# Performance work log

Hardware: AMD Instinct MI355X
Metric: run time of the kernel (lower is better)

## Reference

```python
import jax, jax.numpy as jnp
import numpy as np

INPUT_DIM = 41      # observed channels
D = 2 * INPUT_DIM   # attention value dim (values + mask concat)
E = 128             # embed_time
NH = 1              # num_heads
DK = E // NH
H = 128             # nhidden
NLIN = 50
LAT = 20
B, TK, TQ = 8, 512, 128


def _lin_init(k, out_d, in_d):
    return jax.random.normal(k, (out_d, in_d)) * (1.0 / np.sqrt(in_d))


def setup_inputs() -> dict:
    key = jax.random.key(0)
    ks = jax.random.split(key, 32)
    vals = jax.random.normal(ks[0], (B, TK, INPUT_DIM))
    obs = (jax.random.uniform(ks[1], (B, TK, INPUT_DIM)) > 0.3).astype(jnp.float32)
    x = jnp.concatenate([vals * obs, obs], axis=-1)          # [B,TK,2*INPUT_DIM]
    time_steps = jnp.sort(jax.random.uniform(ks[2], (B, TK)), axis=1)
    query = jnp.linspace(0.0, 1.0, TQ)                        # reference time points
    inp = dict(x=x, time_steps=time_steps, query=query)
    # learned time embedders (mtan_time_embedder): Linear(1,1) + Linear(1,E-1)
    inp['e1_wp'] = jax.random.normal(ks[3], (E - 1,)); inp['e1_bp'] = jax.random.normal(ks[4], (E - 1,)) * 0.1
    inp['e1_wl'] = jax.random.normal(ks[5], (1,));     inp['e1_bl'] = jax.random.normal(ks[6], (1,)) * 0.1
    inp['e2_wp'] = jax.random.normal(ks[7], (E - 1,)); inp['e2_bp'] = jax.random.normal(ks[8], (E - 1,)) * 0.1
    inp['e2_wl'] = jax.random.normal(ks[9], (1,));     inp['e2_bl'] = jax.random.normal(ks[10], (1,)) * 0.1
    # multiTimeAttention linears
    inp['Wq'] = _lin_init(ks[11], E, E); inp['bq'] = jnp.zeros((E,))
    inp['Wk'] = _lin_init(ks[12], E, E); inp['bk'] = jnp.zeros((E,))
    inp['Wo'] = _lin_init(ks[13], H, NH * D); inp['bo'] = jnp.zeros((H,))
    # bidirectional GRU (PyTorch layout: W_ih [3H,in], W_hh [3H,H])
    inp['gwi_f'] = _lin_init(ks[14], 3 * H, H); inp['gwh_f'] = _lin_init(ks[15], 3 * H, H)
    inp['gbi_f'] = jnp.zeros((3 * H,));         inp['gbh_f'] = jnp.zeros((3 * H,))
    inp['gwi_b'] = _lin_init(ks[16], 3 * H, H); inp['gwh_b'] = _lin_init(ks[17], 3 * H, H)
    inp['gbi_b'] = jnp.zeros((3 * H,));         inp['gbh_b'] = jnp.zeros((3 * H,))
    # hiddens_to_z0 MLP
    inp['W1'] = _lin_init(ks[18], NLIN, 2 * H); inp['b1'] = jnp.zeros((NLIN,))
    inp['W2'] = _lin_init(ks[19], 2 * LAT, NLIN); inp['b2'] = jnp.zeros((2 * LAT,))
    return inp


def _time_embed(tt, wp, bp, wl, bl):
    tt = tt[..., None]                               # [...,1]
    out1 = tt * wl + bl                              # [...,1]
    out2 = jnp.sin(tt * wp + bp)                     # [...,E-1]
    return jnp.concatenate([out1, out2], axis=-1)    # [...,E]


def _gru_scan(xs, Wi, Wh, bi, bh):
    # xs: [T,B,in] -> hidden states [T,B,H]; PyTorch GRU equations
    h0 = jnp.zeros((xs.shape[1], Wh.shape[1]), xs.dtype)
    def step(h, xt):
        gi = xt @ Wi.T + bi
        gh = h @ Wh.T + bh
        ir, iz, inn = jnp.split(gi, 3, axis=-1)
        hr, hz, hn = jnp.split(gh, 3, axis=-1)
        r = jax.nn.sigmoid(ir + hr)
        z = jax.nn.sigmoid(iz + hz)
        n = jnp.tanh(inn + r * hn)
        hnew = (1.0 - z) * n + z * h
        return hnew, hnew
    _, ys = jax.lax.scan(step, h0, xs)
    return ys


def reference(x, time_steps, query, e1_wp, e1_bp, e1_wl, e1_bl, e2_wp, e2_bp, e2_wl, e2_bl,
              Wq, bq, Wk, bk, Wo, bo, gwi_f, gwh_f, gbi_f, gbh_f, gwi_b, gwh_b, gbi_b, gbh_b,
              W1, b1, W2, b2):
    b, tk, _ = x.shape
    tq = query.shape[0]
    mask = x[:, :, INPUT_DIM:]                                 # [B,TK,INPUT_DIM]
    mask2 = jnp.concatenate([mask, mask], axis=-1)             # [B,TK,D]
    k_emb = _time_embed(time_steps, e1_wp, e1_bp, e1_wl, e1_bl)   # embedder1(key)   [B,TK,E]
    q_emb = _time_embed(query[None, :], e2_wp, e2_bp, e2_wl, e2_bl)  # embedder2(query) [1,TQ,E]
    q = (q_emb @ Wq.T + bq).reshape(1, tq, NH, DK).transpose(0, 2, 1, 3)   # [1,h,TQ,dk]
    k = (k_emb @ Wk.T + bk).reshape(b, tk, NH, DK).transpose(0, 2, 1, 3)   # [B,h,TK,dk]
    scores = jnp.einsum('ahqd,bhkd->bhqk', q, k) / np.sqrt(DK)             # [B,h,TQ,TK]
    # per-channel masked softmax over keys (the blown-up 5D tensor in the original)
    s5 = jnp.where(mask2[:, None, None, :, :] == 0, -1e9, scores[..., None])  # [B,h,TQ,TK,D]
    p = jax.nn.softmax(s5, axis=-2)
    att = jnp.einsum('bhqkd,bkd->bhqd', p, x)                  # value = x; [B,h,TQ,D]
    att = att.transpose(0, 2, 1, 3).reshape(b, tq, NH * D)
    out = att @ Wo.T + bo                                      # [B,TQ,H]
    xs = out.transpose(1, 0, 2)                                # [TQ,B,H]
    hf = _gru_scan(xs, gwi_f, gwh_f, gbi_f, gbh_f)
    hb = _gru_scan(xs[::-1], gwi_b, gwh_b, gbi_b, gbh_b)[::-1]
    h = jnp.concatenate([hf, hb], axis=-1).transpose(1, 0, 2)  # [B,TQ,2H]
    z = jax.nn.relu(h @ W1.T + b1) @ W2.T + b2                 # [B,TQ,2*LAT]
    return z
```

## Files before the change

kernel.cpp:

```cpp
#include <hip/hip_runtime.h>
#include <math.h>

#define TKK 512
#define TQQ 128
#define BB  8
#define EE  128
#define DD  82
#define IND 41
#define HH  128
#define G3  384
#define NL  50
#define OD  40

typedef __attribute__((ext_vector_type(8))) short short8v;
typedef __attribute__((ext_vector_type(4))) float f32x4;
#define MFMA16(a, b, c) __builtin_amdgcn_mfma_f32_16x16x32_bf16(a, b, c, 0, 0, 0)
#define RCP(x) __builtin_amdgcn_rcpf(x)

__device__ __forceinline__ short f2bf(float f) {
  unsigned u = __float_as_uint(f);
  unsigned r = (u + 0x7fffu + ((u >> 16) & 1u)) >> 16;
  return (short)r;
}
__device__ __forceinline__ float dot4(float4 a, float4 b) {
  return a.x * b.x + a.y * b.y + a.z * b.z + a.w * b.w;
}

__global__ __launch_bounds__(128) void embed_project(
    const float* __restrict__ time_steps, const float* __restrict__ query,
    const float* __restrict__ e1_wp, const float* __restrict__ e1_bp,
    const float* __restrict__ e1_wl, const float* __restrict__ e1_bl,
    const float* __restrict__ e2_wp, const float* __restrict__ e2_bp,
    const float* __restrict__ e2_wl, const float* __restrict__ e2_bl,
    const float* __restrict__ Wk, const float* __restrict__ bk,
    const float* __restrict__ Wq, const float* __restrict__ bq,
    float* __restrict__ kproj, float* __restrict__ qproj) {
  __shared__ float emb[8][EE];
  int i = blockIdx.x;
  int e = threadIdx.x;
  const float *wp, *bp, *wl, *bl, *W, *bias;
  float* out;
  int row0;
  const float* tsrc;
  if (i < 512) {
    int b = i & 7, rg = i >> 3;
    row0 = b * TKK + rg * 8;
    tsrc = time_steps + row0;
    wp = e1_wp; bp = e1_bp; wl = e1_wl; bl = e1_bl; W = Wk; bias = bk;
    out = kproj + (size_t)row0 * EE;
  } else {
    int qg = i - 512;
    row0 = qg * 8;
    tsrc = query + row0;
    wp = e2_wp; bp = e2_bp; wl = e2_wl; bl = e2_bl; W = Wq; bias = bq;
    out = qproj + (size_t)row0 * EE;
  }
  float wpv = 0.f, bpv = 0.f;
  if (e > 0) { wpv = wp[e - 1]; bpv = bp[e - 1]; }
  float wlv = wl[0], blv = bl[0];
#pragma unroll
  for (int r = 0; r < 8; r++) {
    float t = tsrc[r];
    emb[r][e] = (e == 0) ? (t * wlv + blv) : sinf(t * wpv + bpv);
  }
  __syncthreads();
  const float4* wr4 = (const float4*)(W + (size_t)e * EE);
  const float4* em4 = (const float4*)emb;
  float bv = bias[e];
  float acc[8];
#pragma unroll
  for (int r = 0; r < 8; r++) acc[r] = bv;
#pragma unroll 4
  for (int c = 0; c < 32; c++) {
    float4 wv = wr4[c];
#pragma unroll
    for (int r = 0; r < 8; r++) acc[r] += dot4(wv, em4[r * 32 + c]);
  }
#pragma unroll
  for (int r = 0; r < 8; r++) out[(size_t)r * EE + e] = acc[r];
}

__global__ __launch_bounds__(256) void attention(
    const float* __restrict__ x, const float* __restrict__ kproj,
    const float* __restrict__ qproj, const float* __restrict__ Wo,
    const float* __restrict__ bo,
    const float* __restrict__ gwi_f, const float* __restrict__ gbi_f,
    const float* __restrict__ gwi_b, const float* __restrict__ gbi_b,
    float* __restrict__ gi) {
  __shared__ float qv[4][EE];
  __shared__ float4 w4[TKK];
  __shared__ float red[4][4];
  __shared__ float mfin[4];
  __shared__ float part[2][4][DD];
  __shared__ float numb[4][DD];
  __shared__ float attb[4][DD];
  __shared__ float xsr[4][EE];
  __shared__ float wo_lds[HH * DD];
  int b = blockIdx.x & 7, qg = blockIdx.x >> 3;
  int q0 = qg * 4;
  int tid = threadIdx.x;
  int rq = tid >> 2, ec = tid & 3;

  {
    int idx = tid * 2, qi = idx >> 7, j = idx & 127;
    *(float2*)&qv[qi][j] = *(const float2*)(qproj + (size_t)(q0 + qi) * EE + j);
    const float4* wo4 = (const float4*)Wo;
    float4* wl4 = (float4*)wo_lds;
#pragma unroll
    for (int it = 0; it < 11; it++) {
      int i4 = tid + it * 256;
      if (i4 < HH * DD / 4) wl4[i4] = wo4[i4];
    }
  }
  __syncthreads();

  const float scale = 0.08838834764831845f;
  float lm[4] = {-1e30f, -1e30f, -1e30f, -1e30f};
  const float4* qv4 = (const float4*)qv;
  for (int p = 0; p < 8; p++) {
    int r = p * 64 + rq;
    const float4* kr = (const float4*)(kproj + (size_t)(b * TKK + r) * EE);
    float s[4] = {0.f, 0.f, 0.f, 0.f};
#pragma unroll
    for (int c = 0; c < 8; c++) {
      float4 kv = kr[c * 4 + ec];
#pragma unroll
      for (int qi = 0; qi < 4; qi++) s[qi] += dot4(kv, qv4[qi * 32 + c * 4 + ec]);
    }
#pragma unroll
    for (int qi = 0; qi < 4; qi++) {
      s[qi] += __shfl_xor(s[qi], 1, 64);
      s[qi] += __shfl_xor(s[qi], 2, 64);
      s[qi] *= scale;
      lm[qi] = fmaxf(lm[qi], s[qi]);
    }
    if (ec == 0) { float4 sv = {s[0], s[1], s[2], s[3]}; w4[r] = sv; }
  }
  for (int off = 32; off; off >>= 1)
#pragma unroll
    for (int qi = 0; qi < 4; qi++) lm[qi] = fmaxf(lm[qi], __shfl_xor(lm[qi], off, 64));
  if ((tid & 63) == 0)
#pragma unroll
    for (int qi = 0; qi < 4; qi++) red[tid >> 6][qi] = lm[qi];
  __syncthreads();
  if (tid < 4) {
    float m = red[0][tid];
    for (int w = 1; w < 4; w++) m = fmaxf(m, red[w][tid]);
    mfin[tid] = m;
  }
  __syncthreads();
  {
    float m0 = mfin[0], m1 = mfin[1], m2 = mfin[2], m3 = mfin[3];
    float4 v0 = w4[tid], v1 = w4[256 + tid];
    v0.x = __expf(v0.x - m0); v0.y = __expf(v0.y - m1);
    v0.z = __expf(v0.z - m2); v0.w = __expf(v0.w - m3);
    v1.x = __expf(v1.x - m0); v1.y = __expf(v1.y - m1);
    v1.z = __expf(v1.z - m2); v1.w = __expf(v1.w - m3);
    w4[tid] = v0; w4[256 + tid] = v1;
  }
  __syncthreads();

  if (tid < 2 * DD) {
    int c = (tid >= DD), d = tid - c * DD;
    const float* xp = x + ((size_t)(b * TKK + c * 256)) * DD + d;
    float a0 = 0.f, a1 = 0.f, a2 = 0.f, a3 = 0.f;
#pragma unroll 8
    for (int k = 0; k < 256; k++) {
      float xv = xp[(size_t)k * DD];
      float4 wv = w4[c * 256 + k];
      a0 += wv.x * xv; a1 += wv.y * xv; a2 += wv.z * xv; a3 += wv.w * xv;
    }
    part[c][0][d] = a0; part[c][1][d] = a1; part[c][2][d] = a2; part[c][3][d] = a3;
  }
  __syncthreads();
  if (tid < DD) {
#pragma unroll
    for (int qi = 0; qi < 4; qi++) numb[qi][tid] = part[0][qi][tid] + part[1][qi][tid];
  }
  __syncthreads();
  if (tid < DD) {
    int j = tid % IND;
#pragma unroll
    for (int qi = 0; qi < 4; qi++)
      attb[qi][tid] = numb[qi][tid] * RCP(numb[qi][IND + j]);
  }
  __syncthreads();

  {
    int o = tid & 127, g = tid >> 7;
    const float* wrow = wo_lds + o * DD;
    float acc0 = bo[o], acc1 = acc0;
#pragma unroll 2
    for (int d = 0; d < DD; d++) {
      float wv = wrow[d];
      acc0 += wv * attb[2 * g][d];
      acc1 += wv * attb[2 * g + 1][d];
    }
    xsr[2 * g][o] = acc0;
    xsr[2 * g + 1][o] = acc1;
  }
  __syncthreads();

  const float4* xs4 = (const float4*)xsr;
  for (int p = 0; p < 12; p++) {
    int o = p * 64 + rq;
    int dirn = (o >= G3) ? 1 : 0;
    int oo = o - dirn * G3;
    int gate = oo >> 7, col = oo & 127;
    const float4* wr = (const float4*)((dirn ? gwi_b : gwi_f) + (size_t)oo * EE);
    float a[4] = {0.f, 0.f, 0.f, 0.f};
#pragma unroll
    for (int c = 0; c < 8; c++) {
      float4 wv = wr[c * 4 + ec];
#pragma unroll
      for (int qi = 0; qi < 4; qi++) a[qi] += dot4(wv, xs4[qi * 32 + c * 4 + ec]);
    }
#pragma unroll
    for (int qi = 0; qi < 4; qi++) {
      a[qi] += __shfl_xor(a[qi], 1, 64);
      a[qi] += __shfl_xor(a[qi], 2, 64);
    }
    float bi = (dirn ? gbi_b : gbi_f)[oo];
    if (ec == 0) {
      float* gp = gi + (((size_t)(dirn * BB + b) * TQQ + q0) * HH + col) * 4 + gate;
      gp[0] = a[0] + bi; gp[512] = a[1] + bi; gp[1024] = a[2] + bi; gp[1536] = a[3] + bi;
    }
  }
}

__global__ __launch_bounds__(512, 1) void gru_seq(const float* __restrict__ gi,
                                                  const float* __restrict__ gwh_f,
                                                  const float* __restrict__ gbh_f,
                                                  const float* __restrict__ gwh_b,
                                                  const float* __restrict__ gbh_b,
                                                  float* __restrict__ hcat) {
  __shared__ short hb[2][HH];
  int dir = blockIdx.x >> 3, b = blockIdx.x & 7;
  const float* Wh = dir ? gwh_b : gwh_f;
  const float* bh = dir ? gbh_b : gbh_f;
  int tid = threadIdx.x;
  int w = tid >> 6, l = tid & 63;
  int lhi = l >> 4, llo = l & 15;
  int o = 16 * w + llo;
  bool tl = (lhi == 0);

  for (int i = tid; i < 2 * HH / 2; i += 512) ((int*)hb)[i] = 0;

  short8v Bf[3][4];
#pragma unroll
  for (int g = 0; g < 3; g++) {
    const float* wr = Wh + (size_t)(g * HH + o) * EE;
#pragma unroll
    for (int kk = 0; kk < 4; kk++) {
      int k0 = kk * 32 + lhi * 8;
      short8v v;
#pragma unroll
      for (int i = 0; i < 8; i++) v[i] = f2bf(wr[k0 + i]);
      Bf[g][kk] = v;
    }
  }
  float bhr = bh[o], bhz = bh[HH + o], bhn = bh[2 * HH + o];
  float hprev = 0.f;
  float hst[16];

  float4 g0, g1, g2, g3;
  const size_t dbase = ((size_t)(dir * BB + b) * TQQ) * 512 + (size_t)o * 4;

  auto gi_load = [&](int step, float4& dst) {
    int tt = dir ? (TQQ - 1 - step) : step;
    dst = *(const float4*)(gi + dbase + (size_t)tt * 512);
  };
  __syncthreads();
  gi_load(0, g0); gi_load(1, g1);

  auto body = [&](int step, float4& gc, float4& gn, float& hs) {
    int cur = step & 1;
    const char* hrow = (const char*)&hb[cur][0];
    int ao = lhi * 16;
    short8v A0 = *(const short8v*)(hrow + 0 * 64 + ao);
    short8v A1 = *(const short8v*)(hrow + 1 * 64 + ao);
    short8v A2 = *(const short8v*)(hrow + 2 * 64 + ao);
    short8v A3 = *(const short8v*)(hrow + 3 * 64 + ao);
    { int ls = step + 2; gi_load(ls > TQQ - 1 ? TQQ - 1 : ls, gn); }
    f32x4 z4 = {0.f, 0.f, 0.f, 0.f};
    f32x4 aR = z4, aZ = z4, aN = z4;
    aR = MFMA16(A0, Bf[0][0], aR); aZ = MFMA16(A0, Bf[1][0], aZ); aN = MFMA16(A0, Bf[2][0], aN);
    aR = MFMA16(A1, Bf[0][1], aR); aZ = MFMA16(A1, Bf[1][1], aZ); aN = MFMA16(A1, Bf[2][1], aN);
    aR = MFMA16(A2, Bf[0][2], aR); aZ = MFMA16(A2, Bf[1][2], aZ); aN = MFMA16(A2, Bf[2][2], aN);
    aR = MFMA16(A3, Bf[0][3], aR); aZ = MFMA16(A3, Bf[1][3], aZ); aN = MFMA16(A3, Bf[2][3], aN);
    if (tl) {
      float rp = gc.x + bhr + aR[0];
      float zp = gc.y + bhz + aZ[0];
      float hn = aN[0] + bhn;
      float r = RCP(1.f + __expf(-rp));
      float z = RCP(1.f + __expf(-zp));
      float a = gc.z + r * hn;
      float e = __expf(2.f * a);
      float n = 1.f - 2.f * RCP(1.f + e);
      float hnew = n + z * (hprev - n);
      hprev = hnew;
      hs = hnew;
      hb[cur ^ 1][o] = f2bf(hnew);
    }
    asm volatile("s_waitcnt lgkmcnt(0)" ::: "memory");
    __builtin_amdgcn_s_barrier();
    __builtin_amdgcn_sched_barrier(0);
  };

  for (int so = 0; so < TQQ / 16; so++) {
    int s0i = so * 16;
    body(s0i + 0,  g0, g2, hst[0]);
    body(s0i + 1,  g1, g3, hst[1]);
    body(s0i + 2,  g2, g0, hst[2]);
    body(s0i + 3,  g3, g1, hst[3]);
    body(s0i + 4,  g0, g2, hst[4]);
    body(s0i + 5,  g1, g3, hst[5]);
    body(s0i + 6,  g2, g0, hst[6]);
    body(s0i + 7,  g3, g1, hst[7]);
    body(s0i + 8,  g0, g2, hst[8]);
    body(s0i + 9,  g1, g3, hst[9]);
    body(s0i + 10, g2, g0, hst[10]);
    body(s0i + 11, g3, g1, hst[11]);
    body(s0i + 12, g0, g2, hst[12]);
    body(s0i + 13, g1, g3, hst[13]);
    body(s0i + 14, g2, g0, hst[14]);
    body(s0i + 15, g3, g1, hst[15]);
    if (tl) {
#pragma unroll
      for (int si = 0; si < 16; si++) {
        int step = s0i + si;
        int t = dir ? (TQQ - 1 - step) : step;
        hcat[((size_t)b * TQQ + t) * (2 * HH) + dir * HH + o] = hst[si];
      }
    }
  }
}

__global__ __launch_bounds__(512) void mlp_out(const float* __restrict__ hcat,
                                               const float* __restrict__ W1,
                                               const float* __restrict__ b1,
                                               const float* __restrict__ W2,
                                               const float* __restrict__ b2,
                                               float* __restrict__ out) {
  __shared__ float hrow[8][2 * HH];
  __shared__ float ybuf[8][52];
  int i = blockIdx.x;
  int b = i & 7, tg = i >> 3;
  int tid = threadIdx.x;
  size_t rowbase = (size_t)(b * TQQ + tg * 8) * (2 * HH);
  ((float4*)hrow)[tid] = *(const float4*)(hcat + rowbase + tid * 4);
  __syncthreads();
  int r = tid >> 6, o = tid & 63;
  if (o < NL) {
    const float4* w1 = (const float4*)(W1 + (size_t)o * (2 * HH));
    const float4* h4 = (const float4*)hrow[r];
    float acc = b1[o];
#pragma unroll 8
    for (int c = 0; c < 64; c++) acc += dot4(w1[c], h4[c]);
    ybuf[r][o] = fmaxf(acc, 0.f);
  }
  __syncthreads();
  if (o < OD) {
    const float* w2 = W2 + (size_t)o * NL;
    float acc = b2[o];
#pragma unroll 10
    for (int j = 0; j < NL; j++) acc += w2[j] * ybuf[r][j];
    out[((size_t)(b * TQQ + tg * 8) + r) * OD + o] = acc;
  }
}

extern "C" void kernel_launch(void* const* d_in, const int* in_sizes, int n_in,
                              void* d_out, int out_size, void* d_ws, size_t ws_size,
                              hipStream_t stream) {
  const float* x          = (const float*)d_in[0];
  const float* time_steps = (const float*)d_in[1];
  const float* query      = (const float*)d_in[2];
  const float* e1_wp = (const float*)d_in[3];
  const float* e1_bp = (const float*)d_in[4];
  const float* e1_wl = (const float*)d_in[5];
  const float* e1_bl = (const float*)d_in[6];
  const float* e2_wp = (const float*)d_in[7];
  const float* e2_bp = (const float*)d_in[8];
  const float* e2_wl = (const float*)d_in[9];
  const float* e2_bl = (const float*)d_in[10];
  const float* Wq = (const float*)d_in[11];
  const float* bq = (const float*)d_in[12];
  const float* Wk = (const float*)d_in[13];
  const float* bk = (const float*)d_in[14];
  const float* Wo = (const float*)d_in[15];
  const float* bo = (const float*)d_in[16];
  const float* gwi_f = (const float*)d_in[17];
  const float* gwh_f = (const float*)d_in[18];
  const float* gbi_f = (const float*)d_in[19];
  const float* gbh_f = (const float*)d_in[20];
  const float* gwi_b = (const float*)d_in[21];
  const float* gwh_b = (const float*)d_in[22];
  const float* gbi_b = (const float*)d_in[23];
  const float* gbh_b = (const float*)d_in[24];
  const float* W1 = (const float*)d_in[25];
  const float* b1 = (const float*)d_in[26];
  const float* W2 = (const float*)d_in[27];
  const float* b2 = (const float*)d_in[28];

  float* ws    = (float*)d_ws;
  float* kproj = ws;
  float* qproj = kproj + 4096 * 128;
  float* gi    = qproj + 128 * 128;
  float* hcat  = gi + 16 * 128 * 128 * 4;

  embed_project<<<528, 128, 0, stream>>>(time_steps, query,
                                         e1_wp, e1_bp, e1_wl, e1_bl,
                                         e2_wp, e2_bp, e2_wl, e2_bl,
                                         Wk, bk, Wq, bq, kproj, qproj);
  attention<<<256, 256, 0, stream>>>(x, kproj, qproj, Wo, bo,
                                     gwi_f, gbi_f, gwi_b, gbi_b, gi);
  gru_seq<<<16, 512, 0, stream>>>(gi, gwh_f, gbh_f, gwh_b, gbh_b, hcat);
  mlp_out<<<128, 512, 0, stream>>>(hcat, W1, b1, W2, b2, (float*)d_out);
}
```

Baseline: 104.8 us.

## Double attention block threads and halve GRU waves with two column tiles each

The attention kernel now runs 512 threads per block. Score, value-reduction, output-projection and gate loops are re-split across twice as many threads, and the value reduction is split into four key chunks. The GRU kernel goes from 8 to 4 waves, each wave computing two 16-column MFMA tiles. More lanes do useful gate math, barrier cost per step should drop, and the gi prefetch distance grows to three steps. The trade-off is more registers per wave in the GRU (twice the B fragments) and an extra partial-sum reduction in attention.

Result: faster. 99.84 us (-4.7%).

```diff
diff --git a/kernel.cpp b/kernel.cpp
--- a/kernel.cpp
+++ b/kernel.cpp
@@ -80,7 +80,7 @@
   for (int r = 0; r < 8; r++) out[(size_t)r * EE + e] = acc[r];
 }
 
-__global__ __launch_bounds__(256) void attention(
+__global__ __launch_bounds__(512) void attention(
     const float* __restrict__ x, const float* __restrict__ kproj,
     const float* __restrict__ qproj, const float* __restrict__ Wo,
     const float* __restrict__ bo,
@@ -89,9 +89,9 @@
     float* __restrict__ gi) {
   __shared__ float qv[4][EE];
   __shared__ float4 w4[TKK];
-  __shared__ float red[4][4];
+  __shared__ float red[8][4];
   __shared__ float mfin[4];
-  __shared__ float part[2][4][DD];
+  __shared__ float part[4][4][DD];
   __shared__ float numb[4][DD];
   __shared__ float attb[4][DD];
   __shared__ float xsr[4][EE];
@@ -102,13 +102,12 @@
   int rq = tid >> 2, ec = tid & 3;
 
   {
-    int idx = tid * 2, qi = idx >> 7, j = idx & 127;
-    *(float2*)&qv[qi][j] = *(const float2*)(qproj + (size_t)(q0 + qi) * EE + j);
+    qv[tid >> 7][tid & 127] = qproj[(size_t)(q0 + (tid >> 7)) * EE + (tid & 127)];
     const float4* wo4 = (const float4*)Wo;
     float4* wl4 = (float4*)wo_lds;
 #pragma unroll
-    for (int it = 0; it < 11; it++) {
-      int i4 = tid + it * 256;
+    for (int it = 0; it < 6; it++) {
+      int i4 = tid + it * 512;
       if (i4 < HH * DD / 4) wl4[i4] = wo4[i4];
     }
   }
@@ -117,8 +116,8 @@
   const float scale = 0.08838834764831845f;
   float lm[4] = {-1e30f, -1e30f, -1e30f, -1e30f};
   const float4* qv4 = (const float4*)qv;
-  for (int p = 0; p < 8; p++) {
-    int r = p * 64 + rq;
+  for (int p = 0; p < 4; p++) {
+    int r = p * 128 + rq;
     const float4* kr = (const float4*)(kproj + (size_t)(b * TKK + r) * EE);
     float s[4] = {0.f, 0.f, 0.f, 0.f};
 #pragma unroll
@@ -145,37 +144,39 @@
   __syncthreads();
   if (tid < 4) {
     float m = red[0][tid];
-    for (int w = 1; w < 4; w++) m = fmaxf(m, red[w][tid]);
+#pragma unroll
+    for (int w = 1; w < 8; w++) m = fmaxf(m, red[w][tid]);
     mfin[tid] = m;
   }
   __syncthreads();
   {
     float m0 = mfin[0], m1 = mfin[1], m2 = mfin[2], m3 = mfin[3];
-    float4 v0 = w4[tid], v1 = w4[256 + tid];
+    float4 v0 = w4[tid];
     v0.x = __expf(v0.x - m0); v0.y = __expf(v0.y - m1);
     v0.z = __expf(v0.z - m2); v0.w = __expf(v0.w - m3);
-    v1.x = __expf(v1.x - m0); v1.y = __expf(v1.y - m1);
-    v1.z = __expf(v1.z - m2); v1.w = __expf(v1.w - m3);
-    w4[tid] = v0; w4[256 + tid] = v1;
-  }
-  __syncthreads();
-
-  if (tid < 2 * DD) {
-    int c = (tid >= DD), d = tid - c * DD;
-    const float* xp = x + ((size_t)(b * TKK + c * 256)) * DD + d;
-    float a0 = 0.f, a1 = 0.f, a2 = 0.f, a3 = 0.f;
+    w4[tid] = v0;
+  }
+  __syncthreads();
+
+  {
+    int c2 = tid >> 7, d = tid & 127;
+    if (d < DD) {
+      const float* xp = x + ((size_t)(b * TKK + c2 * 128)) * DD + d;
+      float a0 = 0.f, a1 = 0.f, a2 = 0.f, a3 = 0.f;
 #pragma unroll 8
-    for (int k = 0; k < 256; k++) {
-      float xv = xp[(size_t)k * DD];
-      float4 wv = w4[c * 256 + k];
-      a0 += wv.x * xv; a1 += wv.y * xv; a2 += wv.z * xv; a3 += wv.w * xv;
-    }
-    part[c][0][d] = a0; part[c][1][d] = a1; part[c][2][d] = a2; part[c][3][d] = a3;
+      for (int k = 0; k < 128; k++) {
+        float xv = xp[(size_t)k * DD];
+        float4 wv = w4[c2 * 128 + k];
+        a0 += wv.x * xv; a1 += wv.y * xv; a2 += wv.z * xv; a3 += wv.w * xv;
+      }
+      part[c2][0][d] = a0; part[c2][1][d] = a1; part[c2][2][d] = a2; part[c2][3][d] = a3;
+    }
   }
   __syncthreads();
   if (tid < DD) {
 #pragma unroll
-    for (int qi = 0; qi < 4; qi++) numb[qi][tid] = part[0][qi][tid] + part[1][qi][tid];
+    for (int qi = 0; qi < 4; qi++)
+      numb[qi][tid] = part[0][qi][tid] + part[1][qi][tid] + part[2][qi][tid] + part[3][qi][tid];
   }
   __syncthreads();
   if (tid < DD) {
@@ -189,21 +190,16 @@
   {
     int o = tid & 127, g = tid >> 7;
     const float* wrow = wo_lds + o * DD;
-    float acc0 = bo[o], acc1 = acc0;
+    float acc = bo[o];
 #pragma unroll 2
-    for (int d = 0; d < DD; d++) {
-      float wv = wrow[d];
-      acc0 += wv * attb[2 * g][d];
-      acc1 += wv * attb[2 * g + 1][d];
-    }
-    xsr[2 * g][o] = acc0;
-    xsr[2 * g + 1][o] = acc1;
+    for (int d = 0; d < DD; d++) acc += wrow[d] * attb[g][d];
+    xsr[g][o] = acc;
   }
   __syncthreads();
 
   const float4* xs4 = (const float4*)xsr;
-  for (int p = 0; p < 12; p++) {
-    int o = p * 64 + rq;
+  for (int p = 0; p < 6; p++) {
+    int o = p * 128 + rq;
     int dirn = (o >= G3) ? 1 : 0;
     int oo = o - dirn * G3;
     int gate = oo >> 7, col = oo & 127;
@@ -228,7 +224,7 @@
   }
 }
 
-__global__ __launch_bounds__(512, 1) void gru_seq(const float* __restrict__ gi,
+__global__ __launch_bounds__(256, 1) void gru_seq(const float* __restrict__ gi,
                                                   const float* __restrict__ gwh_f,
                                                   const float* __restrict__ gbh_f,
                                                   const float* __restrict__ gwh_b,
@@ -241,37 +237,43 @@
   int tid = threadIdx.x;
   int w = tid >> 6, l = tid & 63;
   int lhi = l >> 4, llo = l & 15;
-  int o = 16 * w + llo;
-  bool tl = (lhi == 0);
-
-  for (int i = tid; i < 2 * HH / 2; i += 512) ((int*)hb)[i] = 0;
-
-  short8v Bf[3][4];
-#pragma unroll
-  for (int g = 0; g < 3; g++) {
-    const float* wr = Wh + (size_t)(g * HH + o) * EE;
-#pragma unroll
-    for (int kk = 0; kk < 4; kk++) {
-      int k0 = kk * 32 + lhi * 8;
-      short8v v;
-#pragma unroll
-      for (int i = 0; i < 8; i++) v[i] = f2bf(wr[k0 + i]);
-      Bf[g][kk] = v;
-    }
-  }
-  float bhr = bh[o], bhz = bh[HH + o], bhn = bh[2 * HH + o];
+  int col0 = 32 * w + llo, col1 = col0 + 16;
+  bool c0 = (lhi < 2);
+  int o_sel = c0 ? col0 : col1;
+  bool wr_lane = ((lhi & 1) == 0);
+
+  if (tid < HH) { hb[0][tid] = 0; hb[1][tid] = 0; }
+
+  short8v Bf[2][3][4];
+#pragma unroll
+  for (int tj = 0; tj < 2; tj++) {
+    int colt = 32 * w + 16 * tj + llo;
+#pragma unroll
+    for (int g = 0; g < 3; g++) {
+      const float* wrp = Wh + (size_t)(g * HH + colt) * EE;
+#pragma unroll
+      for (int kk = 0; kk < 4; kk++) {
+        int k0 = kk * 32 + lhi * 8;
+        short8v v;
+#pragma unroll
+        for (int i = 0; i < 8; i++) v[i] = f2bf(wrp[k0 + i]);
+        Bf[tj][g][kk] = v;
+      }
+    }
+  }
+  float bhr = bh[o_sel], bhz = bh[HH + o_sel], bhn = bh[2 * HH + o_sel];
   float hprev = 0.f;
   float hst[16];
 
   float4 g0, g1, g2, g3;
-  const size_t dbase = ((size_t)(dir * BB + b) * TQQ) * 512 + (size_t)o * 4;
+  const size_t dbase = ((size_t)(dir * BB + b) * TQQ) * 512 + (size_t)o_sel * 4;
 
   auto gi_load = [&](int step, float4& dst) {
     int tt = dir ? (TQQ - 1 - step) : step;
     dst = *(const float4*)(gi + dbase + (size_t)tt * 512);
   };
   __syncthreads();
-  gi_load(0, g0); gi_load(1, g1);
+  gi_load(0, g0); gi_load(1, g1); gi_load(2, g2);
 
   auto body = [&](int step, float4& gc, float4& gn, float& hs) {
     int cur = step & 1;
@@ -281,27 +283,32 @@
     short8v A1 = *(const short8v*)(hrow + 1 * 64 + ao);
     short8v A2 = *(const short8v*)(hrow + 2 * 64 + ao);
     short8v A3 = *(const short8v*)(hrow + 3 * 64 + ao);
-    { int ls = step + 2; gi_load(ls > TQQ - 1 ? TQQ - 1 : ls, gn); }
+    { int ls = step + 3; gi_load(ls > TQQ - 1 ? TQQ - 1 : ls, gn); }
     f32x4 z4 = {0.f, 0.f, 0.f, 0.f};
-    f32x4 aR = z4, aZ = z4, aN = z4;
-    aR = MFMA16(A0, Bf[0][0], aR); aZ = MFMA16(A0, Bf[1][0], aZ); aN = MFMA16(A0, Bf[2][0], aN);
-    aR = MFMA16(A1, Bf[0][1], aR); aZ = MFMA16(A1, Bf[1][1], aZ); aN = MFMA16(A1, Bf[2][1], aN);
-    aR = MFMA16(A2, Bf[0][2], aR); aZ = MFMA16(A2, Bf[1][2], aZ); aN = MFMA16(A2, Bf[2][2], aN);
-    aR = MFMA16(A3, Bf[0][3], aR); aZ = MFMA16(A3, Bf[1][3], aZ); aN = MFMA16(A3, Bf[2][3], aN);
-    if (tl) {
-      float rp = gc.x + bhr + aR[0];
-      float zp = gc.y + bhz + aZ[0];
-      float hn = aN[0] + bhn;
-      float r = RCP(1.f + __expf(-rp));
-      float z = RCP(1.f + __expf(-zp));
-      float a = gc.z + r * hn;
-      float e = __expf(2.f * a);
-      float n = 1.f - 2.f * RCP(1.f + e);
-      float hnew = n + z * (hprev - n);
-      hprev = hnew;
-      hs = hnew;
-      hb[cur ^ 1][o] = f2bf(hnew);
-    }
+    f32x4 aR0 = z4, aZ0 = z4, aN0 = z4, aR1 = z4, aZ1 = z4, aN1 = z4;
+    aR0 = MFMA16(A0, Bf[0][0][0], aR0); aZ0 = MFMA16(A0, Bf[0][1][0], aZ0); aN0 = MFMA16(A0, Bf[0][2][0], aN0);
+    aR1 = MFMA16(A0, Bf[1][0][0], aR1); aZ1 = MFMA16(A0, Bf[1][1][0], aZ1); aN1 = MFMA16(A0, Bf[1][2][0], aN1);
+    aR0 = MFMA16(A1, Bf[0][0][1], aR0); aZ0 = MFMA16(A1, Bf[0][1][1], aZ0); aN0 = MFMA16(A1, Bf[0][2][1], aN0);
+    aR1 = MFMA16(A1, Bf[1][0][1], aR1); aZ1 = MFMA16(A1, Bf[1][1][1], aZ1); aN1 = MFMA16(A1, Bf[1][2][1], aN1);
+    aR0 = MFMA16(A2, Bf[0][0][2], aR0); aZ0 = MFMA16(A2, Bf[0][1][2], aZ0); aN0 = MFMA16(A2, Bf[0][2][2], aN0);
+    aR1 = MFMA16(A2, Bf[1][0][2], aR1); aZ1 = MFMA16(A2, Bf[1][1][2], aZ1); aN1 = MFMA16(A2, Bf[1][2][2], aN1);
+    aR0 = MFMA16(A3, Bf[0][0][3], aR0); aZ0 = MFMA16(A3, Bf[0][1][3], aZ0); aN0 = MFMA16(A3, Bf[0][2][3], aN0);
+    aR1 = MFMA16(A3, Bf[1][0][3], aR1); aZ1 = MFMA16(A3, Bf[1][1][3], aZ1); aN1 = MFMA16(A3, Bf[1][2][3], aN1);
+    float rs = c0 ? aR0[0] : aR1[0];
+    float zs = c0 ? aZ0[0] : aZ1[0];
+    float ns = c0 ? aN0[0] : aN1[0];
+    float rp = gc.x + bhr + rs;
+    float zp = gc.y + bhz + zs;
+    float hn = ns + bhn;
+    float r = RCP(1.f + __expf(-rp));
+    float z = RCP(1.f + __expf(-zp));
+    float a = gc.z + r * hn;
+    float e = __expf(2.f * a);
+    float n = 1.f - 2.f * RCP(1.f + e);
+    float hnew = n + z * (hprev - n);
+    hprev = hnew;
+    hs = hnew;
+    if (wr_lane) hb[cur ^ 1][o_sel] = f2bf(hnew);
     asm volatile("s_waitcnt lgkmcnt(0)" ::: "memory");
     __builtin_amdgcn_s_barrier();
     __builtin_amdgcn_sched_barrier(0);
@@ -309,28 +316,28 @@
 
   for (int so = 0; so < TQQ / 16; so++) {
     int s0i = so * 16;
-    body(s0i + 0,  g0, g2, hst[0]);
-    body(s0i + 1,  g1, g3, hst[1]);
-    body(s0i + 2,  g2, g0, hst[2]);
-    body(s0i + 3,  g3, g1, hst[3]);
-    body(s0i + 4,  g0, g2, hst[4]);
-    body(s0i + 5,  g1, g3, hst[5]);
-    body(s0i + 6,  g2, g0, hst[6]);
-    body(s0i + 7,  g3, g1, hst[7]);
-    body(s0i + 8,  g0, g2, hst[8]);
-    body(s0i + 9,  g1, g3, hst[9]);
-    body(s0i + 10, g2, g0, hst[10]);
-    body(s0i + 11, g3, g1, hst[11]);
-    body(s0i + 12, g0, g2, hst[12]);
-    body(s0i + 13, g1, g3, hst[13]);
-    body(s0i + 14, g2, g0, hst[14]);
-    body(s0i + 15, g3, g1, hst[15]);
-    if (tl) {
+    body(s0i + 0,  g0, g3, hst[0]);
+    body(s0i + 1,  g1, g0, hst[1]);
+    body(s0i + 2,  g2, g1, hst[2]);
+    body(s0i + 3,  g3, g2, hst[3]);
+    body(s0i + 4,  g0, g3, hst[4]);
+    body(s0i + 5,  g1, g0, hst[5]);
+    body(s0i + 6,  g2, g1, hst[6]);
+    body(s0i + 7,  g3, g2, hst[7]);
+    body(s0i + 8,  g0, g3, hst[8]);
+    body(s0i + 9,  g1, g0, hst[9]);
+    body(s0i + 10, g2, g1, hst[10]);
+    body(s0i + 11, g3, g2, hst[11]);
+    body(s0i + 12, g0, g3, hst[12]);
+    body(s0i + 13, g1, g0, hst[13]);
+    body(s0i + 14, g2, g1, hst[14]);
+    body(s0i + 15, g3, g2, hst[15]);
+    if (wr_lane) {
 #pragma unroll
       for (int si = 0; si < 16; si++) {
         int step = s0i + si;
         int t = dir ? (TQQ - 1 - step) : step;
-        hcat[((size_t)b * TQQ + t) * (2 * HH) + dir * HH + o] = hst[si];
+        hcat[((size_t)b * TQQ + t) * (2 * HH) + dir * HH + o_sel] = hst[si];
       }
     }
   }
@@ -412,8 +419,8 @@
                                          e1_wp, e1_bp, e1_wl, e1_bl,
                                          e2_wp, e2_bp, e2_wl, e2_bl,
                                          Wk, bk, Wq, bq, kproj, qproj);
-  attention<<<256, 256, 0, stream>>>(x, kproj, qproj, Wo, bo,
+  attention<<<256, 512, 0, stream>>>(x, kproj, qproj, Wo, bo,
                                      gwi_f, gbi_f, gwi_b, gbi_b, gi);
-  gru_seq<<<16, 512, 0, stream>>>(gi, gwh_f, gbh_f, gwh_b, gbh_b, hcat);
+  gru_seq<<<16, 256, 0, stream>>>(gi, gwh_f, gbh_f, gwh_b, gbh_b, hcat);
   mlp_out<<<128, 512, 0, stream>>>(hcat, W1, b1, W2, b2, (float*)d_out);
 }
```

## Store keys, x and GRU input weights in bf16 and widen attention blocks

Applied to the files above, without the earlier changes.

Adds a conversion kernel that casts x and the GRU input weights to bf16, and makes embed_project write the key projections in bf16. The attention kernel now reads these half-width buffers, unpacking to fp32 for the math, and runs 512 threads per block with the key, x and gate loops split across twice as many threads. The aim is to cut global memory traffic in the attention stage and raise parallelism per block. The cost is an extra kernel launch plus a full pass over x every call, and reduced precision in scores and gate inputs.

New measurement: 106.6 us. No clear change (+1.8%).

```diff
diff --git a/kernel.cpp b/kernel.cpp
--- a/kernel.cpp
+++ b/kernel.cpp
@@ -22,8 +22,25 @@
   unsigned r = (u + 0x7fffu + ((u >> 16) & 1u)) >> 16;
   return (short)r;
 }
+__device__ __forceinline__ float bl(unsigned u) { return __uint_as_float(u << 16); }
+__device__ __forceinline__ float bh(unsigned u) { return __uint_as_float(u & 0xffff0000u); }
 __device__ __forceinline__ float dot4(float4 a, float4 b) {
   return a.x * b.x + a.y * b.y + a.z * b.z + a.w * b.w;
+}
+
+__global__ __launch_bounds__(512) void to_bf16(const float* __restrict__ x,
+                                               const float* __restrict__ gwi_f,
+                                               const float* __restrict__ gwi_b,
+                                               unsigned short* __restrict__ x_bf,
+                                               unsigned short* __restrict__ gwi_bf) {
+  int idx = blockIdx.x * 512 + threadIdx.x;
+  if (idx < 335872) {
+    x_bf[idx] = (unsigned short)f2bf(x[idx]);
+  } else {
+    int j = idx - 335872;
+    float v = (j < 49152) ? gwi_f[j] : gwi_b[j - 49152];
+    gwi_bf[j] = (unsigned short)f2bf(v);
+  }
 }
 
 __global__ __launch_bounds__(128) void embed_project(
@@ -34,26 +51,24 @@
     const float* __restrict__ e2_wl, const float* __restrict__ e2_bl,
     const float* __restrict__ Wk, const float* __restrict__ bk,
     const float* __restrict__ Wq, const float* __restrict__ bq,
-    float* __restrict__ kproj, float* __restrict__ qproj) {
+    unsigned short* __restrict__ kproj_bf, float* __restrict__ qproj) {
   __shared__ float emb[8][EE];
   int i = blockIdx.x;
   int e = threadIdx.x;
   const float *wp, *bp, *wl, *bl, *W, *bias;
-  float* out;
   int row0;
   const float* tsrc;
-  if (i < 512) {
+  bool kside = (i < 512);
+  if (kside) {
     int b = i & 7, rg = i >> 3;
     row0 = b * TKK + rg * 8;
     tsrc = time_steps + row0;
     wp = e1_wp; bp = e1_bp; wl = e1_wl; bl = e1_bl; W = Wk; bias = bk;
-    out = kproj + (size_t)row0 * EE;
   } else {
     int qg = i - 512;
     row0 = qg * 8;
     tsrc = query + row0;
     wp = e2_wp; bp = e2_bp; wl = e2_wl; bl = e2_bl; W = Wq; bias = bq;
-    out = qproj + (size_t)row0 * EE;
   }
   float wpv = 0.f, bpv = 0.f;
   if (e > 0) { wpv = wp[e - 1]; bpv = bp[e - 1]; }
@@ -76,22 +91,29 @@
 #pragma unroll
     for (int r = 0; r < 8; r++) acc[r] += dot4(wv, em4[r * 32 + c]);
   }
-#pragma unroll
-  for (int r = 0; r < 8; r++) out[(size_t)r * EE + e] = acc[r];
-}
-
-__global__ __launch_bounds__(256) void attention(
-    const float* __restrict__ x, const float* __restrict__ kproj,
+  if (kside) {
+#pragma unroll
+    for (int r = 0; r < 8; r++)
+      kproj_bf[(size_t)(row0 + r) * EE + e] = (unsigned short)f2bf(acc[r]);
+  } else {
+#pragma unroll
+    for (int r = 0; r < 8; r++) qproj[(size_t)(row0 + r) * EE + e] = acc[r];
+  }
+}
+
+__global__ __launch_bounds__(512) void attention(
+    const unsigned short* __restrict__ x_bf,
+    const unsigned short* __restrict__ kproj_bf,
     const float* __restrict__ qproj, const float* __restrict__ Wo,
     const float* __restrict__ bo,
-    const float* __restrict__ gwi_f, const float* __restrict__ gbi_f,
-    const float* __restrict__ gwi_b, const float* __restrict__ gbi_b,
+    const unsigned short* __restrict__ gwi_bf,
+    const float* __restrict__ gbi_f, const float* __restrict__ gbi_b,
     float* __restrict__ gi) {
   __shared__ float qv[4][EE];
   __shared__ float4 w4[TKK];
-  __shared__ float red[4][4];
+  __shared__ float red[8][4];
   __shared__ float mfin[4];
-  __shared__ float part[2][4][DD];
+  __shared__ float part[4][4][DD];
   __shared__ float numb[4][DD];
   __shared__ float attb[4][DD];
   __shared__ float xsr[4][EE];
@@ -102,13 +124,12 @@
   int rq = tid >> 2, ec = tid & 3;
 
   {
-    int idx = tid * 2, qi = idx >> 7, j = idx & 127;
-    *(float2*)&qv[qi][j] = *(const float2*)(qproj + (size_t)(q0 + qi) * EE + j);
+    qv[tid >> 7][tid & 127] = qproj[(size_t)(q0 + (tid >> 7)) * EE + (tid & 127)];
     const float4* wo4 = (const float4*)Wo;
     float4* wl4 = (float4*)wo_lds;
 #pragma unroll
-    for (int it = 0; it < 11; it++) {
-      int i4 = tid + it * 256;
+    for (int it = 0; it < 6; it++) {
+      int i4 = tid + it * 512;
       if (i4 < HH * DD / 4) wl4[i4] = wo4[i4];
     }
   }
@@ -117,15 +138,23 @@
   const float scale = 0.08838834764831845f;
   float lm[4] = {-1e30f, -1e30f, -1e30f, -1e30f};
   const float4* qv4 = (const float4*)qv;
-  for (int p = 0; p < 8; p++) {
-    int r = p * 64 + rq;
-    const float4* kr = (const float4*)(kproj + (size_t)(b * TKK + r) * EE);
+  for (int p = 0; p < 4; p++) {
+    int r = p * 128 + rq;
+    const uint4* kr = (const uint4*)(kproj_bf + (size_t)(b * TKK + r) * EE);
     float s[4] = {0.f, 0.f, 0.f, 0.f};
 #pragma unroll
-    for (int c = 0; c < 8; c++) {
-      float4 kv = kr[c * 4 + ec];
-#pragma unroll
-      for (int qi = 0; qi < 4; qi++) s[qi] += dot4(kv, qv4[qi * 32 + c * 4 + ec]);
+    for (int c = 0; c < 4; c++) {
+      int c4e = c * 4 + ec;
+      uint4 kv = kr[c4e];
+      float f0 = bl(kv.x), f1 = bh(kv.x), f2 = bl(kv.y), f3 = bh(kv.y);
+      float f4 = bl(kv.z), f5 = bh(kv.z), f6 = bl(kv.w), f7 = bh(kv.w);
+#pragma unroll
+      for (int qi = 0; qi < 4; qi++) {
+        float4 qa = qv4[qi * 32 + c4e * 2];
+        float4 qb = qv4[qi * 32 + c4e * 2 + 1];
+        s[qi] += f0 * qa.x + f1 * qa.y + f2 * qa.z + f3 * qa.w +
+                 f4 * qb.x + f5 * qb.y + f6 * qb.z + f7 * qb.w;
+      }
     }
 #pragma unroll
     for (int qi = 0; qi < 4; qi++) {
@@ -145,37 +174,39 @@
   __syncthreads();
   if (tid < 4) {
     float m = red[0][tid];
-    for (int w = 1; w < 4; w++) m = fmaxf(m, red[w][tid]);
+#pragma unroll
+    for (int w = 1; w < 8; w++) m = fmaxf(m, red[w][tid]);
     mfin[tid] = m;
   }
   __syncthreads();
   {
     float m0 = mfin[0], m1 = mfin[1], m2 = mfin[2], m3 = mfin[3];
-    float4 v0 = w4[tid], v1 = w4[256 + tid];
+    float4 v0 = w4[tid];
     v0.x = __expf(v0.x - m0); v0.y = __expf(v0.y - m1);
     v0.z = __expf(v0.z - m2); v0.w = __expf(v0.w - m3);
-    v1.x = __expf(v1.x - m0); v1.y = __expf(v1.y - m1);
-    v1.z = __expf(v1.z - m2); v1.w = __expf(v1.w - m3);
-    w4[tid] = v0; w4[256 + tid] = v1;
-  }
-  __syncthreads();
-
-  if (tid < 2 * DD) {
-    int c = (tid >= DD), d = tid - c * DD;
-    const float* xp = x + ((size_t)(b * TKK + c * 256)) * DD + d;
-    float a0 = 0.f, a1 = 0.f, a2 = 0.f, a3 = 0.f;
+    w4[tid] = v0;
+  }
+  __syncthreads();
+
+  {
+    int c2 = tid >> 7, d = tid & 127;
+    if (d < DD) {
+      const unsigned short* xp = x_bf + ((size_t)(b * TKK + c2 * 128)) * DD + d;
+      float a0 = 0.f, a1 = 0.f, a2 = 0.f, a3 = 0.f;
 #pragma unroll 8
-    for (int k = 0; k < 256; k++) {
-      float xv = xp[(size_t)k * DD];
-      float4 wv = w4[c * 256 + k];
-      a0 += wv.x * xv; a1 += wv.y * xv; a2 += wv.z * xv; a3 += wv.w * xv;
-    }
-    part[c][0][d] = a0; part[c][1][d] = a1; part[c][2][d] = a2; part[c][3][d] = a3;
+      for (int k = 0; k < 128; k++) {
+        float xv = __uint_as_float(((unsigned)xp[(size_t)k * DD]) << 16);
+        float4 wv = w4[c2 * 128 + k];
+        a0 += wv.x * xv; a1 += wv.y * xv; a2 += wv.z * xv; a3 += wv.w * xv;
+      }
+      part[c2][0][d] = a0; part[c2][1][d] = a1; part[c2][2][d] = a2; part[c2][3][d] = a3;
+    }
   }
   __syncthreads();
   if (tid < DD) {
 #pragma unroll
-    for (int qi = 0; qi < 4; qi++) numb[qi][tid] = part[0][qi][tid] + part[1][qi][tid];
+    for (int qi = 0; qi < 4; qi++)
+      numb[qi][tid] = part[0][qi][tid] + part[1][qi][tid] + part[2][qi][tid] + part[3][qi][tid];
   }
   __syncthreads();
   if (tid < DD) {
@@ -189,31 +220,34 @@
   {
     int o = tid & 127, g = tid >> 7;
     const float* wrow = wo_lds + o * DD;
-    float acc0 = bo[o], acc1 = acc0;
+    float acc = bo[o];
 #pragma unroll 2
-    for (int d = 0; d < DD; d++) {
-      float wv = wrow[d];
-      acc0 += wv * attb[2 * g][d];
-      acc1 += wv * attb[2 * g + 1][d];
-    }
-    xsr[2 * g][o] = acc0;
-    xsr[2 * g + 1][o] = acc1;
+    for (int d = 0; d < DD; d++) acc += wrow[d] * attb[g][d];
+    xsr[g][o] = acc;
   }
   __syncthreads();
 
   const float4* xs4 = (const float4*)xsr;
-  for (int p = 0; p < 12; p++) {
-    int o = p * 64 + rq;
+  for (int p = 0; p < 6; p++) {
+    int o = p * 128 + rq;
     int dirn = (o >= G3) ? 1 : 0;
     int oo = o - dirn * G3;
     int gate = oo >> 7, col = oo & 127;
-    const float4* wr = (const float4*)((dirn ? gwi_b : gwi_f) + (size_t)oo * EE);
+    const uint4* wr = (const uint4*)(gwi_bf + (size_t)dirn * 49152 + (size_t)oo * EE);
     float a[4] = {0.f, 0.f, 0.f, 0.f};
 #pragma unroll
-    for (int c = 0; c < 8; c++) {
-      float4 wv = wr[c * 4 + ec];
-#pragma unroll
-      for (int qi = 0; qi < 4; qi++) a[qi] += dot4(wv, xs4[qi * 32 + c * 4 + ec]);
+    for (int c = 0; c < 4; c++) {
+      int c4e = c * 4 + ec;
+      uint4 wv = wr[c4e];
+      float f0 = bl(wv.x), f1 = bh(wv.x), f2 = bl(wv.y), f3 = bh(wv.y);
+      float f4 = bl(wv.z), f5 = bh(wv.z), f6 = bl(wv.w), f7 = bh(wv.w);
+#pragma unroll
+      for (int qi = 0; qi < 4; qi++) {
+        float4 qa = xs4[qi * 32 + c4e * 2];
+        float4 qb = xs4[qi * 32 + c4e * 2 + 1];
+        a[qi] += f0 * qa.x + f1 * qa.y + f2 * qa.z + f3 * qa.w +
+                 f4 * qb.x + f5 * qb.y + f6 * qb.z + f7 * qb.w;
+      }
     }
 #pragma unroll
     for (int qi = 0; qi < 4; qi++) {
@@ -403,17 +437,20 @@
   const float* b2 = (const float*)d_in[28];
 
   float* ws    = (float*)d_ws;
-  float* kproj = ws;
-  float* qproj = kproj + 4096 * 128;
-  float* gi    = qproj + 128 * 128;
-  float* hcat  = gi + 16 * 128 * 128 * 4;
-
+  float* qproj = ws;
+  float* gi    = qproj + 16384;
+  float* hcat  = gi + 1048576;
+  unsigned short* kproj_bf = (unsigned short*)(hcat + 262144);
+  unsigned short* x_bf     = kproj_bf + 524288;
+  unsigned short* gwi_bf   = x_bf + 335872;
+
+  to_bf16<<<848, 512, 0, stream>>>(x, gwi_f, gwi_b, x_bf, gwi_bf);
   embed_project<<<528, 128, 0, stream>>>(time_steps, query,
                                          e1_wp, e1_bp, e1_wl, e1_bl,
                                          e2_wp, e2_bp, e2_wl, e2_bl,
-                                         Wk, bk, Wq, bq, kproj, qproj);
-  attention<<<256, 256, 0, stream>>>(x, kproj, qproj, Wo, bo,
-                                     gwi_f, gbi_f, gwi_b, gbi_b, gi);
+                                         Wk, bk, Wq, bq, kproj_bf, qproj);
+  attention<<<256, 512, 0, stream>>>(x_bf, kproj_bf, qproj, Wo, bo,
+                                     gwi_bf, gbi_f, gbi_b, gi);
   gru_seq<<<16, 512, 0, stream>>>(gi, gwh_f, gbh_f, gwh_b, gbh_b, hcat);
   mlp_out<<<128, 512, 0, stream>>>(hcat, W1, b1, W2, b2, (float*)d_out);
 }
```
